# Kernel tuning notes

Measured on AMD Instinct MI355X. Metric: run time of the kernel, lower is better.

Reference implementation:

```python
import jax, jax.numpy as jnp
import numpy as np

D_MODEL = 768
N_HEAD = 12
BATCH = 2
SEQ = 2048
MASK_FILL = -100000.0


def setup_inputs() -> dict:
    key = jax.random.key(0)
    ks = jax.random.split(key, 10)
    s = 1.0 / np.sqrt(D_MODEL)
    inp = {
        "xEnc": jax.random.normal(ks[0], (BATCH, SEQ, D_MODEL), jnp.float32),
        "xDec": jax.random.normal(ks[1], (BATCH, SEQ, D_MODEL), jnp.float32),
        # causal mask: True where attention is disallowed (j > i)
        "mask": (jnp.arange(SEQ)[None, :] > jnp.arange(SEQ)[:, None])[None, None, :, :],
        "wQ": jax.random.uniform(ks[2], (D_MODEL, D_MODEL), jnp.float32, -s, s),
        "bQ": jax.random.uniform(ks[3], (D_MODEL,), jnp.float32, -s, s),
        "wK": jax.random.uniform(ks[4], (D_MODEL, D_MODEL), jnp.float32, -s, s),
        "bK": jax.random.uniform(ks[5], (D_MODEL,), jnp.float32, -s, s),
        "wV": jax.random.uniform(ks[6], (D_MODEL, D_MODEL), jnp.float32, -s, s),
        "bV": jax.random.uniform(ks[7], (D_MODEL,), jnp.float32, -s, s),
        "wOut": jax.random.uniform(ks[8], (D_MODEL, D_MODEL), jnp.float32, -s, s),
        "bOut": jax.random.uniform(ks[9], (D_MODEL,), jnp.float32, -s, s),
    }
    return inp


def reference(xEnc, xDec, mask, wQ, bQ, wK, bK, wV, bV, wOut, bOut):
    B, S, D = xEnc.shape
    H = N_HEAD
    Dh = D // H
    # torch Linear: y = x @ W.T + b
    Q = xDec @ wQ.T + bQ
    K = xEnc @ wK.T + bK
    V = xEnc @ wV.T + bV
    Q = Q.reshape(B, S, H, Dh).transpose(0, 2, 1, 3)  # [B,H,S,Dh]
    K = K.reshape(B, S, H, Dh).transpose(0, 2, 1, 3)
    V = V.reshape(B, S, H, Dh).transpose(0, 2, 1, 3)
    score = jnp.einsum("bhqd,bhkd->bhqk", Q, K) / jnp.sqrt(jnp.float32(Dh))
    score = jnp.where(mask, MASK_FILL, score)
    attn = jax.nn.softmax(score, axis=-1)
    ctx = jnp.einsum("bhqk,bhkd->bhqd", attn, V)  # [B,H,S,Dh]
    ctx = ctx.transpose(0, 2, 1, 3).reshape(B, S, D)
    return ctx @ wOut.T + bOut
```

## Files before the change

### kernel.cpp

```cpp
#include <hip/hip_runtime.h>
#include <stdint.h>
#include <stddef.h>

#define DMODEL 768
#define NHEAD 12
#define SEQLEN 2048
#define NBATCH 2
#define DH 64
#define MTOT (NBATCH*SEQLEN)

typedef short s16x4 __attribute__((ext_vector_type(4)));
typedef short s16x8 __attribute__((ext_vector_type(8)));
typedef float f32x4 __attribute__((ext_vector_type(4)));

#define XDECB_OFF 0u
#define XENCB_OFF 3145728u
#define WQB_OFF   6291456u
#define WKB_OFF   6881280u
#define WVB_OFF   7471104u
#define WOUTB_OFF 8060928u
#define QB_OFF    8650752u
#define KB_OFF    11796480u
#define VT_OFF    14942208u
#define CTXB_OFF  18087936u

#define QSCALE 0.18033688011112042f

static __device__ __forceinline__ unsigned short f2bf(float f) {
  union { float f; unsigned int u; } v; v.f = f;
  unsigned int r = v.u + 0x7fffu + ((v.u >> 16) & 1u);
  return (unsigned short)(r >> 16);
}

static __device__ __forceinline__ unsigned int pack2bf(float f0, float f1) {
  union { float f; unsigned int u; } a, b; a.f = f0; b.f = f1;
  return __builtin_amdgcn_perm(b.u + 0x8000u, a.u + 0x8000u, 0x07060302u);
}

#if __has_builtin(__builtin_amdgcn_exp2f)
#define EXP2(x) __builtin_amdgcn_exp2f(x)
#else
#define EXP2(x) exp2f(x)
#endif

static __device__ __forceinline__ f32x4 mfma16(s16x4 a, s16x4 b, f32x4 c) {
  return __builtin_amdgcn_mfma_f32_16x16x16bf16_1k(a, b, c, 0, 0, 0);
}
static __device__ __forceinline__ f32x4 mfma32(s16x8 a, s16x8 b, f32x4 c) {
  return __builtin_amdgcn_mfma_f32_16x16x32_bf16(a, b, c, 0, 0, 0);
}

typedef __attribute__((address_space(3))) unsigned int lds_u32_t;
typedef const __attribute__((address_space(1))) unsigned int glb_u32_t;
static __device__ __forceinline__ void gl_lds16(const unsigned short* g,
                                                unsigned short* l) {
  __builtin_amdgcn_global_load_lds((glb_u32_t*)g, (lds_u32_t*)l, 16, 0, 0);
}

__global__ __launch_bounds__(256) void cvt_kernel(
    const float* __restrict__ xDec, const float* __restrict__ xEnc,
    const float* __restrict__ wQ, const float* __restrict__ wK,
    const float* __restrict__ wV, const float* __restrict__ wOut,
    unsigned short* __restrict__ ws)
{
  const int seg = blockIdx.y;
  const float* src;
  unsigned int n4, off;
  switch (seg) {
    case 0:  src = xDec; n4 = 786432; off = XDECB_OFF; break;
    case 1:  src = xEnc; n4 = 786432; off = XENCB_OFF; break;
    case 2:  src = wQ;   n4 = 147456; off = WQB_OFF;   break;
    case 3:  src = wK;   n4 = 147456; off = WKB_OFF;   break;
    case 4:  src = wV;   n4 = 147456; off = WVB_OFF;   break;
    default: src = wOut; n4 = 147456; off = WOUTB_OFF; break;
  }
  unsigned short* d = ws + off;
  const unsigned int stride = gridDim.x * blockDim.x;
  for (unsigned int i = blockIdx.x * blockDim.x + threadIdx.x; i < n4; i += stride) {
    const float4 v = ((const float4*)src)[i];
    s16x4 p;
    p[0] = (short)f2bf(v.x); p[1] = (short)f2bf(v.y);
    p[2] = (short)f2bf(v.z); p[3] = (short)f2bf(v.w);
    ((s16x4*)d)[i] = p;
  }
}

#define BK 64

__global__ __launch_bounds__(256, 6) void qkv_gemm(
    const unsigned short* __restrict__ xDecB, const unsigned short* __restrict__ xEncB,
    const unsigned short* __restrict__ wQB, const unsigned short* __restrict__ wKB,
    const unsigned short* __restrict__ wVB,
    const float* __restrict__ bQ, const float* __restrict__ bK, const float* __restrict__ bV,
    unsigned short* __restrict__ Qb, unsigned short* __restrict__ Kb,
    unsigned short* __restrict__ Vt)
{
  const int z = blockIdx.z;
  const unsigned short* __restrict__ A = (z == 0) ? xDecB : xEncB;
  const unsigned short* __restrict__ B = (z == 0) ? wQB : ((z == 1) ? wKB : wVB);
  const float* __restrict__ bias = (z == 0) ? bQ : ((z == 1) ? bK : bV);

  __shared__ unsigned short lA[64 * BK];
  __shared__ unsigned short lB[64 * BK];

  const int tid  = threadIdx.x;
  const int lane = tid & 63;
  const int wid  = tid >> 6;
  const int ln   = lane & 15;
  const int qd   = lane >> 4;
  const int m0 = blockIdx.x * 64;
  const int n0 = blockIdx.y * 64;
  const int wm = (wid & 1) * 32;
  const int wn = (wid >> 1) * 32;

  int srow[2], scol[2];
  #pragma unroll
  for (int c = 0; c < 2; ++c) {
    const int s = c * 256 + wid * 64 + lane;
    srow[c] = s >> 3;
    scol[c] = (((s & 7) ^ ((s >> 3) & 7)) * 8);
  }

  f32x4 acc[2][2] = {};

  for (int k0 = 0; k0 < DMODEL; k0 += BK) {
    #pragma unroll
    for (int c = 0; c < 2; ++c) {
      const int ldsoff = (c * 256 + wid * 64) * 8;
      gl_lds16(A + (size_t)(m0 + srow[c]) * DMODEL + k0 + scol[c], &lA[ldsoff]);
      gl_lds16(B + (size_t)(n0 + srow[c]) * DMODEL + k0 + scol[c], &lB[ldsoff]);
    }
    __syncthreads();
    #pragma unroll
    for (int kc = 0; kc < 2; ++kc) {
      s16x8 af[2], bfr[2];
      #pragma unroll
      for (int i = 0; i < 2; ++i) {
        const int r = wm + i * 16 + ln;
        af[i] = *(const s16x8*)&lA[r * 64 + (((kc * 4 + qd) ^ (r & 7)) * 8)];
      }
      #pragma unroll
      for (int j = 0; j < 2; ++j) {
        const int r = wn + j * 16 + ln;
        bfr[j] = *(const s16x8*)&lB[r * 64 + (((kc * 4 + qd) ^ (r & 7)) * 8)];
      }
      #pragma unroll
      for (int i = 0; i < 2; ++i)
        #pragma unroll
        for (int j = 0; j < 2; ++j)
          acc[i][j] = mfma32(af[i], bfr[j], acc[i][j]);
    }
    __syncthreads();
  }

  #pragma unroll
  for (int j = 0; j < 2; ++j) {
    const int n_g = n0 + wn + j * 16 + ln;
    const float bv = bias[n_g];
    const int h    = n_g >> 6;
    const int dcol = n_g & 63;
    #pragma unroll
    for (int i = 0; i < 2; ++i) {
      #pragma unroll
      for (int r = 0; r < 4; ++r) {
        const int m_g  = m0 + wm + i * 16 + qd * 4 + r;
        const int bb   = m_g >> 11;
        const int srow2 = m_g & 2047;
        const float val = acc[i][j][r] + bv;
        if (z == 0)
          Qb[((size_t)((bb * NHEAD + h) * SEQLEN + srow2)) * DH + dcol] = f2bf(val * QSCALE);
        else if (z == 1)
          Kb[((size_t)((bb * NHEAD + h) * SEQLEN + srow2)) * DH + dcol] = f2bf(val);
        else
          Vt[((size_t)((bb * NHEAD + h) * DH + dcol)) * SEQLEN + srow2] = f2bf(val);
      }
    }
  }
}

__global__ __launch_bounds__(256, 6) void out_gemm(
    const unsigned short* __restrict__ ctx, const unsigned short* __restrict__ wOutB,
    const float* __restrict__ bOut, float* __restrict__ out)
{
  __shared__ unsigned short lA[64 * BK];
  __shared__ unsigned short lB[64 * BK];

  const int tid  = threadIdx.x;
  const int lane = tid & 63;
  const int wid  = tid >> 6;
  const int ln   = lane & 15;
  const int qd   = lane >> 4;
  const int m0 = blockIdx.x * 64;
  const int n0 = blockIdx.y * 64;
  const int wm = (wid & 1) * 32;
  const int wn = (wid >> 1) * 32;

  int srow[2], scol[2];
  #pragma unroll
  for (int c = 0; c < 2; ++c) {
    const int s = c * 256 + wid * 64 + lane;
    srow[c] = s >> 3;
    scol[c] = (((s & 7) ^ ((s >> 3) & 7)) * 8);
  }

  f32x4 acc[2][2] = {};

  for (int k0 = 0; k0 < DMODEL; k0 += BK) {
    #pragma unroll
    for (int c = 0; c < 2; ++c) {
      const int ldsoff = (c * 256 + wid * 64) * 8;
      gl_lds16(ctx + (size_t)(m0 + srow[c]) * DMODEL + k0 + scol[c], &lA[ldsoff]);
      gl_lds16(wOutB + (size_t)(n0 + srow[c]) * DMODEL + k0 + scol[c], &lB[ldsoff]);
    }
    __syncthreads();
    #pragma unroll
    for (int kc = 0; kc < 2; ++kc) {
      s16x8 af[2], bfr[2];
      #pragma unroll
      for (int i = 0; i < 2; ++i) {
        const int r = wm + i * 16 + ln;
        af[i] = *(const s16x8*)&lA[r * 64 + (((kc * 4 + qd) ^ (r & 7)) * 8)];
      }
      #pragma unroll
      for (int j = 0; j < 2; ++j) {
        const int r = wn + j * 16 + ln;
        bfr[j] = *(const s16x8*)&lB[r * 64 + (((kc * 4 + qd) ^ (r & 7)) * 8)];
      }
      #pragma unroll
      for (int i = 0; i < 2; ++i)
        #pragma unroll
        for (int j = 0; j < 2; ++j)
          acc[i][j] = mfma32(af[i], bfr[j], acc[i][j]);
    }
    __syncthreads();
  }

  #pragma unroll
  for (int j = 0; j < 2; ++j) {
    const int n_g = n0 + wn + j * 16 + ln;
    const float bv = bOut[n_g];
    #pragma unroll
    for (int i = 0; i < 2; ++i) {
      #pragma unroll
      for (int r = 0; r < 4; ++r) {
        const int m_g = m0 + wm + i * 16 + qd * 4 + r;
        out[(size_t)m_g * DMODEL + n_g] = acc[i][j][r] + bv;
      }
    }
  }
}

#define KVT 128
#define LKP 72
#define LVP 136

__global__ __launch_bounds__(256, 3) void attn_kernel(
    const unsigned short* __restrict__ Qb, const unsigned short* __restrict__ Kb,
    const unsigned short* __restrict__ Vt, unsigned short* __restrict__ ctx,
    float* __restrict__ pout0, float* __restrict__ pout1,
    float* __restrict__ lpart)
{
  __shared__ unsigned short lK[KVT * LKP];
  __shared__ unsigned short lV[DH * LVP];

  const int tid  = threadIdx.x;
  const int lane = tid & 63;
  const int wid  = tid >> 6;
  const int ln   = lane & 15;
  const int qd   = lane >> 4;
  const int bh = blockIdx.y;
  const int p  = blockIdx.x;
  const bool isA = p < 16;
  const int i  = isA ? p : (p - 16);
  const int Ti = (i + 2) >> 1;

  const unsigned short* Kbase = Kb + (size_t)bh * SEQLEN * DH;
  const unsigned short* Vbase = Vt + (size_t)bh * DH * SEQLEN;
  const int bb = bh / NHEAD;
  const int h  = bh % NHEAD;

  auto run = [&](int q0, int t0, int nt, int mode) {
    const int q_lane = q0 + wid * 16 + ln;
    s16x8 qf[2];
    {
      const unsigned short* Qrow = Qb + ((size_t)bh * SEQLEN + q_lane) * DH;
      qf[0] = *(const s16x8*)(Qrow + qd * 8);
      qf[1] = *(const s16x8*)(Qrow + 32 + qd * 8);
    }
    float l_run = 0.0f;
    f32x4 o_acc[4] = {};

    s16x8 rK[4], rV[4];
    auto load_kv = [&](int kv0) {
      #pragma unroll
      for (int c = 0; c < 4; ++c) {
        const int f = tid + c * 256;
        rK[c] = *(const s16x8*)(Kbase + (size_t)(kv0 + (f >> 3)) * DH + (f & 7) * 8);
      }
      #pragma unroll
      for (int c = 0; c < 4; ++c) {
        const int f = tid + c * 256;
        rV[c] = *(const s16x8*)(Vbase + (size_t)(f >> 4) * SEQLEN + kv0 + (f & 15) * 8);
      }
    };

    load_kv(t0 * KVT);
    for (int t = t0; t < t0 + nt; ++t) {
      const int kv0 = t * KVT;
      #pragma unroll
      for (int c = 0; c < 4; ++c) {
        const int f = tid + c * 256;
        *(s16x8*)&lK[(f >> 3) * LKP + (f & 7) * 8] = rK[c];
      }
      #pragma unroll
      for (int c = 0; c < 4; ++c) {
        const int f = tid + c * 256;
        *(s16x8*)&lV[(f >> 4) * LVP + (f & 15) * 8] = rV[c];
      }
      __syncthreads();
      if (t + 1 < t0 + nt) load_kv(kv0 + KVT);

      f32x4 s_acc[8] = {};
      #pragma unroll
      for (int kc = 0; kc < 2; ++kc) {
        #pragma unroll
        for (int t8 = 0; t8 < 8; ++t8) {
          const s16x8 a = *(const s16x8*)&lK[(t8 * 16 + ln) * LKP + kc * 32 + qd * 8];
          s_acc[t8] = mfma32(a, qf[kc], s_acc[t8]);
        }
      }

      if (kv0 + KVT > q0) {
        #pragma unroll
        for (int t8 = 0; t8 < 8; ++t8) {
          #pragma unroll
          for (int r = 0; r < 4; ++r) {
            const int kv = kv0 + t8 * 16 + qd * 4 + r;
            s_acc[t8][r] = (kv > q_lane) ? -1e30f : s_acc[t8][r];
          }
        }
      }

      s16x4 pf[8];
      #pragma unroll
      for (int t8 = 0; t8 < 8; ++t8) {
        const float p0 = EXP2(s_acc[t8][0]);
        const float p1 = EXP2(s_acc[t8][1]);
        const float p2 = EXP2(s_acc[t8][2]);
        const float p3 = EXP2(s_acc[t8][3]);
        l_run += (p0 + p1) + (p2 + p3);
        union { unsigned int u[2]; s16x4 v; } pk;
        pk.u[0] = pack2bf(p0, p1);
        pk.u[1] = pack2bf(p2, p3);
        pf[t8] = pk.v;
      }

      #pragma unroll
      for (int t8 = 0; t8 < 8; ++t8) {
        #pragma unroll
        for (int j = 0; j < 4; ++j) {
          const s16x4 b = *(const s16x4*)&lV[(j * 16 + ln) * LVP + t8 * 16 + qd * 4];
          o_acc[j] = mfma16(pf[t8], b, o_acc[j]);
        }
      }
      __syncthreads();
    }

    l_run += __shfl_xor(l_run, 16);
    l_run += __shfl_xor(l_run, 32);

    if (mode == 0) {
      #pragma unroll
      for (int r = 0; r < 4; ++r) {
        const float lr  = __shfl(l_run, qd * 4 + r);
        const float inv = 1.0f / lr;
        const int q_g = q0 + wid * 16 + qd * 4 + r;
        unsigned short* dst = ctx + ((size_t)bb * SEQLEN + q_g) * DMODEL + h * DH;
        #pragma unroll
        for (int j = 0; j < 4; ++j)
          dst[j * 16 + ln] = f2bf(o_acc[j][r] * inv);
      }
    } else {
      float* PO = (mode == 1) ? pout1 : pout0;
      float* LO = lpart + ((mode == 1) ? (24 * 1024) : 0);
      const int qbase = q0 - 1024 + wid * 16;
      if (lane < 16)
        LO[bh * 1024 + qbase + lane] = l_run;
      #pragma unroll
      for (int j = 0; j < 4; ++j)
        #pragma unroll
        for (int r = 0; r < 4; ++r)
          PO[((size_t)bh * 1024 + qbase + qd * 4 + r) * 64 + j * 16 + ln] =
              o_acc[j][r];
    }
  };

  if (isA) {
    run(i * 64, 0, Ti, 0);
    run((31 - i) * 64, 0, 9 - Ti, 1);
  } else {
    run((31 - i) * 64, 9 - Ti, 8, 2);
  }
}

__global__ __launch_bounds__(256) void norm_kernel(
    const float* __restrict__ pout0, const float* __restrict__ pout1,
    const float* __restrict__ lpart, unsigned short* __restrict__ ctx)
{
  const int e4  = blockIdx.x * 256 + threadIdx.x;
  const int d4  = e4 & 15;
  const int row = e4 >> 4;
  const int bh  = row >> 10;
  const int qr  = row & 1023;
  const float l = lpart[row] + lpart[24 * 1024 + row];
  const float inv = 1.0f / l;
  const float4 a = ((const float4*)pout0)[e4];
  const float4 b = ((const float4*)pout1)[e4];
  const int bb = bh / NHEAD;
  const int h  = bh % NHEAD;
  unsigned short* dst =
      ctx + ((size_t)bb * SEQLEN + 1024 + qr) * DMODEL + h * DH + d4 * 4;
  s16x4 o;
  o[0] = (short)f2bf((a.x + b.x) * inv);
  o[1] = (short)f2bf((a.y + b.y) * inv);
  o[2] = (short)f2bf((a.z + b.z) * inv);
  o[3] = (short)f2bf((a.w + b.w) * inv);
  *(s16x4*)dst = o;
}

extern "C" void kernel_launch(void* const* d_in, const int* in_sizes, int n_in,
                              void* d_out, int out_size, void* d_ws, size_t ws_size,
                              hipStream_t stream)
{
  const float* xEnc = (const float*)d_in[0];
  const float* xDec = (const float*)d_in[1];
  const float* wQ   = (const float*)d_in[3];
  const float* bQ   = (const float*)d_in[4];
  const float* wK   = (const float*)d_in[5];
  const float* bK   = (const float*)d_in[6];
  const float* wV   = (const float*)d_in[7];
  const float* bV   = (const float*)d_in[8];
  const float* wOut = (const float*)d_in[9];
  const float* bOut = (const float*)d_in[10];

  unsigned short* ws = (unsigned short*)d_ws;
  float* pout0 = (float*)(ws + XDECB_OFF);
  float* pout1 = (float*)(ws + XENCB_OFF);
  float* lpart = (float*)(ws + WQB_OFF);

  cvt_kernel<<<dim3(512, 6), 256, 0, stream>>>(xDec, xEnc, wQ, wK, wV, wOut, ws);
  qkv_gemm<<<dim3(MTOT / 64, DMODEL / 64, 3), 256, 0, stream>>>(
      ws + XDECB_OFF, ws + XENCB_OFF, ws + WQB_OFF, ws + WKB_OFF, ws + WVB_OFF,
      bQ, bK, bV, ws + QB_OFF, ws + KB_OFF, ws + VT_OFF);
  attn_kernel<<<dim3(32, NBATCH * NHEAD), 256, 0, stream>>>(
      ws + QB_OFF, ws + KB_OFF, ws + VT_OFF, ws + CTXB_OFF,
      pout0, pout1, lpart);
  norm_kernel<<<dim3((24 * 1024 * 16) / 256), 256, 0, stream>>>(
      pout0, pout1, lpart, ws + CTXB_OFF);
  out_gemm<<<dim3(MTOT / 64, DMODEL / 64), 256, 0, stream>>>(
      ws + CTXB_OFF, ws + WOUTB_OFF, bOut, (float*)d_out);
}
```

Baseline: 184.1 us.

## Double-buffer LDS tiles in QKV and output projection GEMMs

```diff
diff --git a/kernel.cpp b/kernel.cpp
--- a/kernel.cpp
+++ b/kernel.cpp
@@ -86,8 +86,9 @@
 }
 
 #define BK 64
-
-__global__ __launch_bounds__(256, 6) void qkv_gemm(
+#define NKT (DMODEL / BK)
+
+__global__ __launch_bounds__(256, 5) void qkv_gemm(
     const unsigned short* __restrict__ xDecB, const unsigned short* __restrict__ xEncB,
     const unsigned short* __restrict__ wQB, const unsigned short* __restrict__ wKB,
     const unsigned short* __restrict__ wVB,
@@ -100,8 +101,8 @@
   const unsigned short* __restrict__ B = (z == 0) ? wQB : ((z == 1) ? wKB : wVB);
   const float* __restrict__ bias = (z == 0) ? bQ : ((z == 1) ? bK : bV);
 
-  __shared__ unsigned short lA[64 * BK];
-  __shared__ unsigned short lB[64 * BK];
+  __shared__ unsigned short lA[2][64 * BK];
+  __shared__ unsigned short lB[2][64 * BK];
 
   const int tid  = threadIdx.x;
   const int lane = tid & 63;
@@ -121,28 +122,34 @@
     scol[c] = (((s & 7) ^ ((s >> 3) & 7)) * 8);
   }
 
-  f32x4 acc[2][2] = {};
-
-  for (int k0 = 0; k0 < DMODEL; k0 += BK) {
+  auto stage = [&](int buf, int k0) {
     #pragma unroll
     for (int c = 0; c < 2; ++c) {
       const int ldsoff = (c * 256 + wid * 64) * 8;
-      gl_lds16(A + (size_t)(m0 + srow[c]) * DMODEL + k0 + scol[c], &lA[ldsoff]);
-      gl_lds16(B + (size_t)(n0 + srow[c]) * DMODEL + k0 + scol[c], &lB[ldsoff]);
-    }
-    __syncthreads();
+      gl_lds16(A + (size_t)(m0 + srow[c]) * DMODEL + k0 + scol[c], &lA[buf][ldsoff]);
+      gl_lds16(B + (size_t)(n0 + srow[c]) * DMODEL + k0 + scol[c], &lB[buf][ldsoff]);
+    }
+  };
+
+  f32x4 acc[2][2] = {};
+
+  stage(0, 0);
+  __syncthreads();
+  int cur = 0;
+  for (int t = 0; t < NKT; ++t) {
+    if (t + 1 < NKT) stage(cur ^ 1, (t + 1) * BK);
     #pragma unroll
     for (int kc = 0; kc < 2; ++kc) {
       s16x8 af[2], bfr[2];
       #pragma unroll
       for (int i = 0; i < 2; ++i) {
         const int r = wm + i * 16 + ln;
-        af[i] = *(const s16x8*)&lA[r * 64 + (((kc * 4 + qd) ^ (r & 7)) * 8)];
+        af[i] = *(const s16x8*)&lA[cur][r * 64 + (((kc * 4 + qd) ^ (r & 7)) * 8)];
       }
       #pragma unroll
       for (int j = 0; j < 2; ++j) {
         const int r = wn + j * 16 + ln;
-        bfr[j] = *(const s16x8*)&lB[r * 64 + (((kc * 4 + qd) ^ (r & 7)) * 8)];
+        bfr[j] = *(const s16x8*)&lB[cur][r * 64 + (((kc * 4 + qd) ^ (r & 7)) * 8)];
       }
       #pragma unroll
       for (int i = 0; i < 2; ++i)
@@ -151,6 +158,7 @@
           acc[i][j] = mfma32(af[i], bfr[j], acc[i][j]);
     }
     __syncthreads();
+    cur ^= 1;
   }
 
   #pragma unroll
@@ -178,12 +186,12 @@
   }
 }
 
-__global__ __launch_bounds__(256, 6) void out_gemm(
+__global__ __launch_bounds__(256, 5) void out_gemm(
     const unsigned short* __restrict__ ctx, const unsigned short* __restrict__ wOutB,
     const float* __restrict__ bOut, float* __restrict__ out)
 {
-  __shared__ unsigned short lA[64 * BK];
-  __shared__ unsigned short lB[64 * BK];
+  __shared__ unsigned short lA[2][64 * BK];
+  __shared__ unsigned short lB[2][64 * BK];
 
   const int tid  = threadIdx.x;
   const int lane = tid & 63;
@@ -203,28 +211,34 @@
     scol[c] = (((s & 7) ^ ((s >> 3) & 7)) * 8);
   }
 
-  f32x4 acc[2][2] = {};
-
-  for (int k0 = 0; k0 < DMODEL; k0 += BK) {
+  auto stage = [&](int buf, int k0) {
     #pragma unroll
     for (int c = 0; c < 2; ++c) {
       const int ldsoff = (c * 256 + wid * 64) * 8;
-      gl_lds16(ctx + (size_t)(m0 + srow[c]) * DMODEL + k0 + scol[c], &lA[ldsoff]);
-      gl_lds16(wOutB + (size_t)(n0 + srow[c]) * DMODEL + k0 + scol[c], &lB[ldsoff]);
-    }
-    __syncthreads();
+      gl_lds16(ctx + (size_t)(m0 + srow[c]) * DMODEL + k0 + scol[c], &lA[buf][ldsoff]);
+      gl_lds16(wOutB + (size_t)(n0 + srow[c]) * DMODEL + k0 + scol[c], &lB[buf][ldsoff]);
+    }
+  };
+
+  f32x4 acc[2][2] = {};
+
+  stage(0, 0);
+  __syncthreads();
+  int cur = 0;
+  for (int t = 0; t < NKT; ++t) {
+    if (t + 1 < NKT) stage(cur ^ 1, (t + 1) * BK);
     #pragma unroll
     for (int kc = 0; kc < 2; ++kc) {
       s16x8 af[2], bfr[2];
       #pragma unroll
       for (int i = 0; i < 2; ++i) {
         const int r = wm + i * 16 + ln;
-        af[i] = *(const s16x8*)&lA[r * 64 + (((kc * 4 + qd) ^ (r & 7)) * 8)];
+        af[i] = *(const s16x8*)&lA[cur][r * 64 + (((kc * 4 + qd) ^ (r & 7)) * 8)];
       }
       #pragma unroll
       for (int j = 0; j < 2; ++j) {
         const int r = wn + j * 16 + ln;
-        bfr[j] = *(const s16x8*)&lB[r * 64 + (((kc * 4 + qd) ^ (r & 7)) * 8)];
+        bfr[j] = *(const s16x8*)&lB[cur][r * 64 + (((kc * 4 + qd) ^ (r & 7)) * 8)];
       }
       #pragma unroll
       for (int i = 0; i < 2; ++i)
@@ -233,6 +247,7 @@
           acc[i][j] = mfma32(af[i], bfr[j], acc[i][j]);
     }
     __syncthreads();
+    cur ^= 1;
   }
 
   #pragma unroll
```

After: 196.8 us. +6.9%, slower.
